# Kernel optimization log

Measured on AMD Instinct MI355X. Metric: run time of the kernel, lower is better.

Reference implementation:

```python
import jax, jax.numpy as jnp
import numpy as np

NUM_HEADS = 8
S = 8192
D = 64          # PROJECTION_WIDTH
WORD_WIDTH = 512  # NUM_HEADS * D


def setup_inputs() -> dict:
    key = jax.random.key(0)
    kq, kk, kv, kw = jax.random.split(key, 4)
    q = jax.random.normal(kq, (S, D), dtype=jnp.float32)
    k = jax.random.normal(kk, (S, D), dtype=jnp.float32)
    v = jax.random.normal(kv, (S, D), dtype=jnp.float32)
    w_o = jax.random.normal(kw, (NUM_HEADS * D, WORD_WIDTH), dtype=jnp.float32)
    return {"q": q, "k": k, "v": v, "w_o": w_o}


def reference(q, k, v, w_o):
    # q_dot_k = q @ k.T / sqrt(d); softmax over dim=1 (rows); no mask.
    scale = 1.0 / jnp.sqrt(jnp.asarray(q.shape[1], dtype=q.dtype))
    scores = jnp.einsum('sd,td->st', q, k) * scale          # [S, S]
    attn = jax.nn.softmax(scores, axis=1)                   # [S, S]
    head = jnp.einsum('st,td->sd', attn, v)                 # [S, D]
    # All NUM_HEADS SelfAttentionLayers share the same (q,k,v) and have no
    # per-head parameters, so concatenating the heads is a tile of one head.
    concat = jnp.tile(head, (1, NUM_HEADS))                 # [S, NUM_HEADS*D]
    return concat @ w_o                                     # [S, WORD_WIDTH]
```

## Files before the change

### kernel.cpp

```cpp
#include <hip/hip_runtime.h>
#include <hip/hip_bf16.h>

typedef _Float16 half8 __attribute__((ext_vector_type(8)));
typedef __fp16 fp16x2 __attribute__((ext_vector_type(2)));
typedef __attribute__((ext_vector_type(4))) float floatx4;
typedef __attribute__((ext_vector_type(2))) float floatx2;
typedef __attribute__((ext_vector_type(2))) unsigned int uint2v;

#define MFMAH(a, b, c) __builtin_amdgcn_mfma_f32_16x16x32_f16((a), (b), (c), 0, 0, 0)

#define SEQ 8192
#define SCALE_LOG2E 0.18033688011112042f

__device__ __forceinline__ unsigned pkh(float a, float b) {
    union { fp16x2 h; unsigned u; } cv;
    cv.h = __builtin_amdgcn_cvt_pkrtz(a, b);
    return cv.u;
}
__device__ __forceinline__ void gload16(const void* gptr, void* lptr) {
    __builtin_amdgcn_global_load_lds(
        (const __attribute__((address_space(1))) void*)gptr,
        (__attribute__((address_space(3))) void*)lptr, 16, 0, 0);
}
__device__ __forceinline__ void block_barrier() {
    asm volatile("" ::: "memory");
    __builtin_amdgcn_s_barrier();
    asm volatile("" ::: "memory");
}

__global__ __launch_bounds__(256) void prep_kernel(
        const float* __restrict__ kg, const float* __restrict__ vg,
        const float* __restrict__ w_o, _Float16* __restrict__ kf,
        _Float16* __restrict__ vt, float* __restrict__ weff) {
    const int bid = blockIdx.x, tid = threadIdx.x;
    if (bid < 256) {
        int e = (bid * 256 + tid) * 8;
        floatx4 a = *(const floatx4*)(kg + e);
        floatx4 b = *(const floatx4*)(kg + e + 4);
        half8 h;
        h[0] = (_Float16)a[0]; h[1] = (_Float16)a[1]; h[2] = (_Float16)a[2]; h[3] = (_Float16)a[3];
        h[4] = (_Float16)b[0]; h[5] = (_Float16)b[1]; h[6] = (_Float16)b[2]; h[7] = (_Float16)b[3];
        *(half8*)(kf + e) = h;
    } else if (bid < 384) {
        __shared__ _Float16 T[64][72];
        const int t0 = (bid - 256) * 64;
        {
            int r = tid >> 2, cs = (tid & 3) * 16;
            const float* vp = vg + (size_t)(t0 + r) * 64 + cs;
            half8 h0, h1;
#pragma unroll
            for (int j = 0; j < 8; ++j) { h0[j] = (_Float16)vp[j]; h1[j] = (_Float16)vp[8 + j]; }
            *(half8*)&T[r][cs] = h0;
            *(half8*)&T[r][cs + 8] = h1;
        }
        __syncthreads();
        {
            int d = tid >> 2, ts = (tid & 3) * 16;
            half8 o0, o1;
#pragma unroll
            for (int j = 0; j < 8; ++j) { o0[j] = T[ts + j][d]; o1[j] = T[ts + 8 + j][d]; }
            *(half8*)(vt + (size_t)d * SEQ + t0 + ts) = o0;
            *(half8*)(vt + (size_t)d * SEQ + t0 + ts + 8) = o1;
        }
    } else {
        int idx = (bid - 384) * 256 + tid;
        int d = idx >> 9, j = idx & 511;
        float s = 0.f;
#pragma unroll
        for (int h = 0; h < 8; ++h) s += w_o[((h * 64 + d) << 9) + j];
        weff[idx] = s;
    }
}

__global__ __launch_bounds__(256, 2) void flash_kernel(
        const float* __restrict__ qg, const _Float16* __restrict__ kf,
        const _Float16* __restrict__ vt, float* __restrict__ pacc,
        float* __restrict__ pm, float* __restrict__ pl, int kvlen) {
    __shared__ __align__(16) char smem[51200];
    _Float16* PTbase = (_Float16*)(smem + 32768);

    const int tid  = threadIdx.x;
    const int lane = tid & 63;
    const int w    = tid >> 6;
    const int l15  = lane & 15;
    const int kgi  = lane >> 4;
    const int qbase = blockIdx.x * 128;
    const int split = blockIdx.y;
    const int kv0   = split * kvlen;
    const int nt    = kvlen >> 6;

    const int r0 = tid >> 3;
    const int g8 = (((tid & 7) ^ (r0 & 7)) << 3);

    auto STAGE = [&](int bsel, int kvb) {
        char* b = smem + bsel * 16384;
        const size_t ko = (size_t)(kvb + r0) * 64 + g8;
        const size_t vo = (size_t)r0 * SEQ + kvb + g8;
        gload16(kf + ko,                    b + tid * 16);
        gload16(kf + ko + 32 * 64,          b + 4096  + tid * 16);
        gload16(vt + vo,                    b + 8192  + tid * 16);
        gload16(vt + vo + (size_t)32 * SEQ, b + 12288 + tid * 16);
    };

    const float* qp = qg + (size_t)(qbase + w * 32 + l15) * 64 + kgi * 8;
    floatx4 qv[2][2][2];
#pragma unroll
    for (int qf = 0; qf < 2; ++qf)
#pragma unroll
        for (int kc = 0; kc < 2; ++kc) {
            qv[qf][kc][0] = *(const floatx4*)(qp + qf * 16 * 64 + kc * 32);
            qv[qf][kc][1] = *(const floatx4*)(qp + qf * 16 * 64 + kc * 32 + 4);
        }

    STAGE(0, kv0);
    STAGE(1, kv0 + 64);

    half8 qh[2][2];
#pragma unroll
    for (int qf = 0; qf < 2; ++qf)
#pragma unroll
        for (int kc = 0; kc < 2; ++kc) {
            half8 h;
#pragma unroll
            for (int i = 0; i < 4; ++i) {
                h[i]     = (_Float16)(qv[qf][kc][0][i] * SCALE_LOG2E);
                h[i + 4] = (_Float16)(qv[qf][kc][1][i] * SCALE_LOG2E);
            }
            qh[qf][kc] = h;
        }

    floatx4 acc[2][4];
#pragma unroll
    for (int qf = 0; qf < 2; ++qf)
#pragma unroll
        for (int i = 0; i < 4; ++i) acc[qf][i] = (floatx4){0.f, 0.f, 0.f, 0.f};
    float m_r[2] = {-1e30f, -1e30f}, l_r[2] = {0.f, 0.f};

    asm volatile("s_waitcnt vmcnt(4)" ::: "memory");
    block_barrier();

    for (int t = 0; t < nt; ++t) {
        const _Float16* KL = (const _Float16*)(smem + (t & 1) * 16384);
        const _Float16* VL = KL + 4096;

        floatx4 st[2][4];
#pragma unroll
        for (int qf = 0; qf < 2; ++qf)
#pragma unroll
            for (int ct = 0; ct < 4; ++ct) st[qf][ct] = (floatx4){0.f, 0.f, 0.f, 0.f};
#pragma unroll
        for (int ct = 0; ct < 4; ++ct) {
            const int row = ct * 16 + l15;
#pragma unroll
            for (int kc = 0; kc < 2; ++kc) {
                const int go = (((kc * 4 + kgi) ^ (row & 7)) << 3);
                const half8 kh = *(const half8*)(KL + row * 64 + go);
                st[0][ct] = MFMAH(kh, qh[0][kc], st[0][ct]);
                st[1][ct] = MFMAH(kh, qh[1][kc], st[1][ct]);
            }
        }

#pragma unroll
        for (int qf = 0; qf < 2; ++qf) {
            float tm = st[qf][0][0];
#pragma unroll
            for (int ct = 0; ct < 4; ++ct)
#pragma unroll
                for (int r = 0; r < 4; ++r) tm = fmaxf(tm, st[qf][ct][r]);
            tm = fmaxf(tm, __shfl_xor(tm, 16));
            tm = fmaxf(tm, __shfl_xor(tm, 32));
            if (!__all(tm - m_r[qf] <= 8.0f)) {
                const float nm = fmaxf(m_r[qf], tm);
                const float alpha = __builtin_amdgcn_exp2f(m_r[qf] - nm);
                l_r[qf] *= alpha;
#pragma unroll
                for (int db = 0; db < 4; ++db) acc[qf][db] *= alpha;
                m_r[qf] = nm;
            }
            const float nm = m_r[qf];
            float ps = 0.f;
#pragma unroll
            for (int ct = 0; ct < 4; ++ct)
#pragma unroll
                for (int r = 0; r < 4; ++r) {
                    float p = __builtin_amdgcn_exp2f(st[qf][ct][r] - nm);
                    st[qf][ct][r] = p;
                    ps += p;
                }
            ps += __shfl_xor(ps, 16);
            ps += __shfl_xor(ps, 32);
            l_r[qf] += ps;

            _Float16* PTw = PTbase + (w * 2 + qf) * (16 * 72);
#pragma unroll
            for (int ct = 0; ct < 4; ++ct) {
                uint2v u = {pkh(st[qf][ct][0], st[qf][ct][1]),
                            pkh(st[qf][ct][2], st[qf][ct][3])};
                *(uint2v*)(PTw + l15 * 72 + ct * 16 + kgi * 4) = u;
            }
        }

        {
            _Float16* PT0 = PTbase + (w * 2 + 0) * (16 * 72);
            _Float16* PT1 = PTbase + (w * 2 + 1) * (16 * 72);
#pragma unroll
            for (int kc = 0; kc < 2; ++kc) {
                const half8 pb0 = *(const half8*)(PT0 + l15 * 72 + kc * 32 + kgi * 8);
                const half8 pb1 = *(const half8*)(PT1 + l15 * 72 + kc * 32 + kgi * 8);
#pragma unroll
                for (int db = 0; db < 4; ++db) {
                    const int row = db * 16 + l15;
                    const int go = (((kc * 4 + kgi) ^ (row & 7)) << 3);
                    const half8 va = *(const half8*)(VL + row * 64 + go);
                    acc[0][db] = MFMAH(va, pb0, acc[0][db]);
                    acc[1][db] = MFMAH(va, pb1, acc[1][db]);
                }
            }
        }

        if (t + 1 < nt) {
            block_barrier();
            if (t + 2 < nt) {
                STAGE(t & 1, kv0 + (t + 2) * 64);
                asm volatile("s_waitcnt vmcnt(4)" ::: "memory");
            } else {
                asm volatile("s_waitcnt vmcnt(0)" ::: "memory");
            }
            block_barrier();
        }
    }

    block_barrier();
    float* Tw = (float*)(smem + w * 4352);
#pragma unroll
    for (int qf = 0; qf < 2; ++qf) {
#pragma unroll
        for (int db = 0; db < 4; ++db)
#pragma unroll
            for (int r = 0; r < 4; ++r)
                Tw[l15 * 68 + db * 16 + kgi * 4 + r] = acc[qf][db][r];
        {
            const int qrow = lane >> 2, gg = lane & 3;
            float* orow = pacc + ((size_t)split * SEQ + qbase + w * 32 + qf * 16 + qrow) * 64 + gg * 16;
#pragma unroll
            for (int i = 0; i < 4; ++i)
                *(floatx4*)(orow + i * 4) = *(const floatx4*)&Tw[qrow * 68 + gg * 16 + i * 4];
        }
        if (lane < 16) {
            pm[(size_t)split * SEQ + qbase + w * 32 + qf * 16 + lane] = m_r[qf];
            pl[(size_t)split * SEQ + qbase + w * 32 + qf * 16 + lane] = l_r[qf];
        }
        __builtin_amdgcn_s_barrier();
    }
}

__global__ __launch_bounds__(256) void combineproj_kernel(
        const float* __restrict__ pacc, const float* __restrict__ pm,
        const float* __restrict__ pl, const float* __restrict__ weff,
        float* __restrict__ out, int KS) {
    __shared__ float hlds[16][64];
    const int tid = threadIdx.x;
    const int s0 = blockIdx.x * 16;
    {
        const int row = tid >> 4, d0 = (tid & 15) * 4;
        const int qq = s0 + row;
        float M = -1e30f;
        for (int s2 = 0; s2 < KS; ++s2) M = fmaxf(M, pm[(size_t)s2 * SEQ + qq]);
        floatx4 A = (floatx4){0.f, 0.f, 0.f, 0.f};
        float L = 0.f;
        for (int s2 = 0; s2 < KS; ++s2) {
            const float wgt = __builtin_amdgcn_exp2f(pm[(size_t)s2 * SEQ + qq] - M);
            L += pl[(size_t)s2 * SEQ + qq] * wgt;
            floatx4 pa = *(const floatx4*)&pacc[((size_t)s2 * SEQ + qq) * 64 + d0];
            A += pa * wgt;
        }
        const float inv = 1.0f / L;
        A *= inv;
        *(floatx4*)&hlds[row][d0] = A;
    }
    __syncthreads();
    const int j0 = tid * 2;
    float a0[16], a1[16];
#pragma unroll
    for (int s = 0; s < 16; ++s) { a0[s] = 0.f; a1[s] = 0.f; }
    for (int d4 = 0; d4 < 16; ++d4) {
        floatx2 wv[4];
#pragma unroll
        for (int dd = 0; dd < 4; ++dd)
            wv[dd] = *(const floatx2*)&weff[(size_t)(d4 * 4 + dd) * 512 + j0];
#pragma unroll
        for (int s = 0; s < 16; ++s) {
            floatx4 h = *(const floatx4*)&hlds[s][d4 * 4];
#pragma unroll
            for (int dd = 0; dd < 4; ++dd) {
                a0[s] += h[dd] * wv[dd][0];
                a1[s] += h[dd] * wv[dd][1];
            }
        }
    }
#pragma unroll
    for (int s = 0; s < 16; ++s) {
        floatx2 o = {a0[s], a1[s]};
        *(floatx2*)&out[(size_t)(s0 + s) * 512 + j0] = o;
    }
}

extern "C" void kernel_launch(void* const* d_in, const int* in_sizes, int n_in,
                              void* d_out, int out_size, void* d_ws, size_t ws_size,
                              hipStream_t stream) {
    const float* q   = (const float*)d_in[0];
    const float* k   = (const float*)d_in[1];
    const float* v   = (const float*)d_in[2];
    const float* w_o = (const float*)d_in[3];
    float* out = (float*)d_out;

    const size_t weff_sz = 64 * 512 * sizeof(float);
    const size_t h_sz    = (size_t)SEQ * 64 * sizeof(_Float16);
    auto need = [&](int ks) {
        return weff_sz + 2 * h_sz
               + (size_t)ks * SEQ * 64 * sizeof(float)
               + 2 * (size_t)ks * SEQ * sizeof(float);
    };
    int KS = 1;
    if (ws_size >= need(8)) KS = 8;
    else if (ws_size >= need(4)) KS = 4;
    else if (ws_size >= need(2)) KS = 2;

    char* p = (char*)d_ws;
    float* weff = (float*)p;  p += weff_sz;
    float* pacc = (float*)p;  p += (size_t)KS * SEQ * 64 * sizeof(float);
    float* pm   = (float*)p;  p += (size_t)KS * SEQ * sizeof(float);
    float* pl   = (float*)p;  p += (size_t)KS * SEQ * sizeof(float);
    _Float16* kf = (_Float16*)p;  p += h_sz;
    _Float16* vt = (_Float16*)p;

    prep_kernel<<<dim3(512), dim3(256), 0, stream>>>(k, v, w_o, kf, vt, weff);
    flash_kernel<<<dim3(SEQ / 128, KS), dim3(256), 0, stream>>>(q, kf, vt, pacc, pm, pl, SEQ / KS);
    combineproj_kernel<<<dim3(SEQ / 16), dim3(256), 0, stream>>>(pacc, pm, pl, weff, out, KS);
}
```

Measured before the change: 120.7 us.

## Pass P fragments via cross-lane shuffles instead of LDS, raise occupancy and split count

The softmax probabilities are now packed to fp16 and redistributed into the PV MFMA operand layout with __shfl, so the per-wave P transpose buffer in LDS is gone. Shared memory shrinks from 51200 to 32768 bytes and launch bounds move from 2 to 4 blocks per CU, which lowers the register budget per thread and risks spills. The host also allows 16 KV splits when the workspace is large enough, giving more blocks but more partial results for the combine kernel to merge.

```diff
diff --git a/kernel.cpp b/kernel.cpp
--- a/kernel.cpp
+++ b/kernel.cpp
@@ -5,7 +5,6 @@
 typedef __fp16 fp16x2 __attribute__((ext_vector_type(2)));
 typedef __attribute__((ext_vector_type(4))) float floatx4;
 typedef __attribute__((ext_vector_type(2))) float floatx2;
-typedef __attribute__((ext_vector_type(2))) unsigned int uint2v;
 
 #define MFMAH(a, b, c) __builtin_amdgcn_mfma_f32_16x16x32_f16((a), (b), (c), 0, 0, 0)
 
@@ -72,12 +71,11 @@
     }
 }
 
-__global__ __launch_bounds__(256, 2) void flash_kernel(
+__global__ __launch_bounds__(256, 4) void flash_kernel(
         const float* __restrict__ qg, const _Float16* __restrict__ kf,
         const _Float16* __restrict__ vt, float* __restrict__ pacc,
         float* __restrict__ pm, float* __restrict__ pl, int kvlen) {
-    __shared__ __align__(16) char smem[51200];
-    _Float16* PTbase = (_Float16*)(smem + 32768);
+    __shared__ __align__(16) char smem[32768];
 
     const int tid  = threadIdx.x;
     const int lane = tid & 63;
@@ -136,6 +134,9 @@
         for (int i = 0; i < 4; ++i) acc[qf][i] = (floatx4){0.f, 0.f, 0.f, 0.f};
     float m_r[2] = {-1e30f, -1e30f}, l_r[2] = {0.f, 0.f};
 
+    const int s0l = l15 + ((lane >> 4) & 1) * 32;
+    const bool hisel = (kgi >> 1) != 0;
+
     asm volatile("s_waitcnt vmcnt(4)" ::: "memory");
     block_barrier();
 
@@ -160,6 +161,7 @@
             }
         }
 
+        half8 pbh[2][2];
 #pragma unroll
         for (int qf = 0; qf < 2; ++qf) {
             float tm = st[qf][0][0];
@@ -191,30 +193,40 @@
             ps += __shfl_xor(ps, 32);
             l_r[qf] += ps;
 
-            _Float16* PTw = PTbase + (w * 2 + qf) * (16 * 72);
+            unsigned U0[4], U1[4];
 #pragma unroll
             for (int ct = 0; ct < 4; ++ct) {
-                uint2v u = {pkh(st[qf][ct][0], st[qf][ct][1]),
-                            pkh(st[qf][ct][2], st[qf][ct][3])};
-                *(uint2v*)(PTw + l15 * 72 + ct * 16 + kgi * 4) = u;
-            }
-        }
-
-        {
-            _Float16* PT0 = PTbase + (w * 2 + 0) * (16 * 72);
-            _Float16* PT1 = PTbase + (w * 2 + 1) * (16 * 72);
+                U0[ct] = pkh(st[qf][ct][0], st[qf][ct][1]);
+                U1[ct] = pkh(st[qf][ct][2], st[qf][ct][3]);
+            }
 #pragma unroll
             for (int kc = 0; kc < 2; ++kc) {
-                const half8 pb0 = *(const half8*)(PT0 + l15 * 72 + kc * 32 + kgi * 8);
-                const half8 pb1 = *(const half8*)(PT1 + l15 * 72 + kc * 32 + kgi * 8);
-#pragma unroll
-                for (int db = 0; db < 4; ++db) {
-                    const int row = db * 16 + l15;
-                    const int go = (((kc * 4 + kgi) ^ (row & 7)) << 3);
-                    const half8 va = *(const half8*)(VL + row * 64 + go);
-                    acc[0][db] = MFMAH(va, pb0, acc[0][db]);
-                    acc[1][db] = MFMAH(va, pb1, acc[1][db]);
-                }
+                unsigned a0 = __shfl(U0[2 * kc],     s0l);
+                unsigned b0 = __shfl(U0[2 * kc + 1], s0l);
+                unsigned a1 = __shfl(U1[2 * kc],     s0l);
+                unsigned b1 = __shfl(U1[2 * kc + 1], s0l);
+                unsigned c0 = __shfl(U0[2 * kc],     s0l + 16);
+                unsigned d0 = __shfl(U0[2 * kc + 1], s0l + 16);
+                unsigned c1 = __shfl(U1[2 * kc],     s0l + 16);
+                unsigned d1 = __shfl(U1[2 * kc + 1], s0l + 16);
+                union { unsigned u[4]; half8 h; } pb;
+                pb.u[0] = hisel ? b0 : a0;
+                pb.u[1] = hisel ? b1 : a1;
+                pb.u[2] = hisel ? d0 : c0;
+                pb.u[3] = hisel ? d1 : c1;
+                pbh[qf][kc] = pb.h;
+            }
+        }
+
+#pragma unroll
+        for (int kc = 0; kc < 2; ++kc) {
+#pragma unroll
+            for (int db = 0; db < 4; ++db) {
+                const int row = db * 16 + l15;
+                const int go = (((kc * 4 + kgi) ^ (row & 7)) << 3);
+                const half8 va = *(const half8*)(VL + row * 64 + go);
+                acc[0][db] = MFMAH(va, pbh[0][kc], acc[0][db]);
+                acc[1][db] = MFMAH(va, pbh[1][kc], acc[1][db]);
             }
         }
 
@@ -322,7 +334,8 @@
                + 2 * (size_t)ks * SEQ * sizeof(float);
     };
     int KS = 1;
-    if (ws_size >= need(8)) KS = 8;
+    if (ws_size >= need(16)) KS = 16;
+    else if (ws_size >= need(8)) KS = 8;
     else if (ws_size >= need(4)) KS = 4;
     else if (ws_size >= need(2)) KS = 2;
 
```

Measured after the change: 122.9 us. No clear change (+1.8%).
